# Performance work log

Hardware: AMD Instinct MI355X
Metric: run time of the kernel (lower is better)

Reference implementation:

```python
import jax, jax.numpy as jnp
import numpy as np

K = 5          # k = min(5, min(S, T)) with S = T = 4096
SIGMA = 1.0
EPS_VAR = 1e-08
EPS_LOG = 1e-08


def _entropy(p):
    # sum(-p * log2(clamp(p, 1e-8)), axis=1).mean()
    return jnp.sum(-p * jnp.log2(jnp.clip(p, EPS_LOG, None)), axis=1).mean()


def _pairwise_dist(x):
    # Euclidean cdist via GEMM (matches torch's use_mm_for_euclid path)
    sq = jnp.sum(x * x, axis=1)                       # [N]
    d2 = sq[:, None] + sq[None, :] - 2.0 * (x @ x.T)  # [N, N]
    d2 = jnp.maximum(d2, 0.0)
    # safe sqrt (zero diagonal) — value identical, grad-safe
    return jnp.where(d2 > 0, jnp.sqrt(jnp.where(d2 > 0, d2, 1.0)), 0.0)


def _row_var(block):
    # sqrt(k-th smallest distance per row + eps): max of k smallest
    kth = -jax.lax.top_k(-block, K)[0][:, -1]
    return jnp.sqrt(kth + EPS_VAR)                    # [rows]


def _sim(block, var_row, zero_diag):
    s = jnp.exp(-block / (2.0 * (var_row[:, None] * SIGMA) ** 2))
    if zero_diag:
        n = block.shape[0]
        s = s * (1.0 - jnp.eye(n, dtype=s.dtype))
    return s


def _forward(Feature_all, logit_all, y_source):
    S = y_source.shape[0]
    logit_source = logit_all[:S]
    logit_target = logit_all[S:]

    # cross-entropy on source
    logp = jax.nn.log_softmax(logit_source, axis=1)
    loss_cl = -jnp.take_along_axis(logp, y_source[:, None], axis=1).mean()

    # entropy of target softmax
    loss_ce = _entropy(jax.nn.softmax(logit_target, axis=1))

    # reg_loss_dist
    dist = _pairwise_dist(Feature_all)                # [N, N]
    d_ss = dist[:S, :S]
    d_st = dist[:S, S:]
    d_tt = dist[S:, S:]
    d_ts = dist[S:, :S]

    sim_ss = _sim(d_ss, _row_var(d_ss), True)
    sim_st = _sim(d_st, _row_var(d_st), False)
    sim_tt = _sim(d_tt, _row_var(d_tt), True)
    sim_ts = _sim(d_ts, _row_var(d_ts), False)

    src_intra = jnp.max(sim_ss, axis=1)
    src_inter = jnp.max(sim_st, axis=1)
    tgt_intra = jnp.max(sim_tt, axis=1)
    tgt_inter = jnp.max(sim_ts, axis=1)

    loss_reg = (jnp.abs(src_intra - src_inter).mean()
                + jnp.abs(tgt_intra - tgt_inter).mean())
    return loss_cl, loss_ce, loss_reg


def setup_inputs() -> dict:
    key = jax.random.key(0)
    k1, k2, k3 = jax.random.split(key, 3)
    N, D, C, S = 8192, 256, 65, 4096
    return {
        "Feature_all": jax.random.normal(k1, (N, D), dtype=jnp.float32),
        "logit_all": jax.random.normal(k2, (N, C), dtype=jnp.float32),
        "y_source": jax.random.randint(k3, (S,), 0, C, dtype=jnp.int64
                                       if jax.config.jax_enable_x64 else jnp.int32),
        "device": 0,
    }


def reference(Feature_all, logit_all, y_source, device):
    del device  # torch-specific, ignored
    return _forward(Feature_all, logit_all, y_source)
```

## Files before the change

### kernel.cpp

```cpp
#include <hip/hip_runtime.h>
#include <stdint.h>

#define Nn 8192
#define Dd 256
#define Ss 4096
#define Cc 65

#define TI 128
#define TJ 128
#define BK 32
#define CHUNK 1024
#define NCHUNK (Nn / CHUNK)
#define NJT (CHUNK / TJ)
#define KS (Dd / BK)

#define BIGF 3.0e37f

typedef float f4 __attribute__((ext_vector_type(4)));
typedef __bf16 bf8 __attribute__((ext_vector_type(8)));

__device__ __forceinline__ float wredsum(float v) {
#pragma unroll
  for (int o = 32; o; o >>= 1) v += __shfl_xor(v, o, 64);
  return v;
}
__device__ __forceinline__ float wredmax(float v) {
#pragma unroll
  for (int o = 32; o; o >>= 1) v = fmaxf(v, __shfl_xor(v, o, 64));
  return v;
}

__device__ __forceinline__ unsigned short f2bf(float f) {
  unsigned int u = __float_as_uint(f);
  u = (u + 0x7fffu + ((u >> 16) & 1u)) >> 16;
  return (unsigned short)u;
}

__global__ __launch_bounds__(256) void prep_kernel(const float* __restrict__ X,
                                                   unsigned short* __restrict__ xb,
                                                   float* __restrict__ sqn) {
  int row = blockIdx.x * 4 + (threadIdx.x >> 6);
  int lane = threadIdx.x & 63;
  f4 v = ((const f4*)(X + (size_t)row * Dd))[lane];
  float ss = v[0] * v[0] + v[1] * v[1] + v[2] * v[2] + v[3] * v[3];
  ss = wredsum(ss);
  if (lane == 0) sqn[row] = ss;
  ushort4 o;
  o.x = f2bf(v[0]); o.y = f2bf(v[1]); o.z = f2bf(v[2]); o.w = f2bf(v[3]);
  ((ushort4*)(xb + (size_t)row * Dd))[lane] = o;
}

__device__ __forceinline__ void stage16(const void* g, void* l) {
  __builtin_amdgcn_global_load_lds((__attribute__((address_space(1))) void*)g,
                                   (__attribute__((address_space(3))) void*)l, 16, 0, 0);
}

__global__ __launch_bounds__(256) void dist_kernel(const unsigned short* __restrict__ xb,
                                                   const float* __restrict__ sqn,
                                                   float* __restrict__ top5ws) {
  __shared__ unsigned short ldsA[2][TJ * BK];
  __shared__ unsigned short ldsB[2][TI * BK];

  const int tid = threadIdx.x;
  const int lane = tid & 63;
  const int wv = tid >> 6;
  const int q = lane >> 4;
  const int c = lane & 15;
  const int jw = wv & 1;
  const int iw = wv >> 1;

  const int ib = (blockIdx.x / NCHUNK) * TI;
  const int chunk = blockIdx.x % NCHUNK;
  const int jc0 = chunk * CHUNK;

  const int swz = q ^ ((lane >> 1) & 3);
  const int pr = lane >> 2;
  const int qd = (lane & 3) ^ ((lane >> 3) & 3);
  const int u0 = wv * 2, u1 = wv * 2 + 1;
  const int gcol = qd * 8;

  float top[4][5];
#pragma unroll
  for (int a = 0; a < 4; ++a)
#pragma unroll
    for (int b = 0; b < 5; ++b) top[a][b] = BIGF;

  const int iwbase = ib + iw * 64;

  for (int jt = 0; jt < NJT; ++jt) {
    const int jb = jc0 + jt * TJ;

    f4 acc[4][4];
    f4 z = {0.f, 0.f, 0.f, 0.f};
#pragma unroll
    for (int a = 0; a < 4; ++a)
#pragma unroll
      for (int b2 = 0; b2 < 4; ++b2) acc[a][b2] = z;

    stage16(xb + (size_t)(jb + u0 * 16 + pr) * Dd + gcol, &ldsA[0][u0 * 512]);
    stage16(xb + (size_t)(jb + u1 * 16 + pr) * Dd + gcol, &ldsA[0][u1 * 512]);
    stage16(xb + (size_t)(ib + u0 * 16 + pr) * Dd + gcol, &ldsB[0][u0 * 512]);
    stage16(xb + (size_t)(ib + u1 * 16 + pr) * Dd + gcol, &ldsB[0][u1 * 512]);
    __syncthreads();

#pragma unroll
    for (int ks = 0; ks < KS; ++ks) {
      const int b = ks & 1;
      if (ks + 1 < KS) {
        const int k0 = (ks + 1) * BK;
        stage16(xb + (size_t)(jb + u0 * 16 + pr) * Dd + k0 + gcol, &ldsA[b ^ 1][u0 * 512]);
        stage16(xb + (size_t)(jb + u1 * 16 + pr) * Dd + k0 + gcol, &ldsA[b ^ 1][u1 * 512]);
        stage16(xb + (size_t)(ib + u0 * 16 + pr) * Dd + k0 + gcol, &ldsB[b ^ 1][u0 * 512]);
        stage16(xb + (size_t)(ib + u1 * 16 + pr) * Dd + k0 + gcol, &ldsB[b ^ 1][u1 * 512]);
      }
      bf8 aF[4], bF[4];
#pragma unroll
      for (int rt = 0; rt < 4; ++rt)
        aF[rt] = *(const bf8*)&ldsA[b][(jw * 64 + rt * 16 + c) * 32 + swz * 8];
#pragma unroll
      for (int ct = 0; ct < 4; ++ct)
        bF[ct] = *(const bf8*)&ldsB[b][(iw * 64 + ct * 16 + c) * 32 + swz * 8];
#pragma unroll
      for (int rt = 0; rt < 4; ++rt)
#pragma unroll
        for (int ct = 0; ct < 4; ++ct)
          acc[rt][ct] = __builtin_amdgcn_mfma_f32_16x16x32_bf16(aF[rt], bF[ct], acc[rt][ct], 0, 0, 0);
      __syncthreads();
    }

    const int jrow = jb + jw * 64;
    f4 sq4[4];
#pragma unroll
    for (int rt = 0; rt < 4; ++rt) sq4[rt] = *(const f4*)&sqn[jrow + rt * 16 + q * 4];
    const bool mayDiag = (jrow == iwbase);
#pragma unroll
    for (int ct = 0; ct < 4; ++ct) {
      float t[16];
#pragma unroll
      for (int rt = 0; rt < 4; ++rt)
#pragma unroll
        for (int r = 0; r < 4; ++r)
          t[rt * 4 + r] = fmaf(acc[rt][ct][r], -2.0f, sq4[rt][r]);
      if (mayDiag && ((c >> 2) == q)) t[ct * 4 + (c & 3)] = BIGF;
      float tm = fminf(fminf(fminf(fminf(t[0], t[1]), fminf(t[2], t[3])),
                             fminf(fminf(t[4], t[5]), fminf(t[6], t[7]))),
                       fminf(fminf(fminf(t[8], t[9]), fminf(t[10], t[11])),
                             fminf(fminf(t[12], t[13]), fminf(t[14], t[15]))));
      if (tm < top[ct][4]) {
#pragma unroll
        for (int kk = 0; kk < 16; ++kk) {
          float x = t[kk];
          if (x < top[ct][4]) {
#pragma unroll
            for (int s = 0; s < 4; ++s) {
              float lo = fminf(top[ct][s], x);
              x = fmaxf(top[ct][s], x);
              top[ct][s] = lo;
            }
            top[ct][4] = x;
          }
        }
      }
    }
  }

#pragma unroll
  for (int ct = 0; ct < 4; ++ct) {
    float a0 = top[ct][0], a1 = top[ct][1], a2 = top[ct][2], a3 = top[ct][3], a4 = top[ct][4];
#pragma unroll
    for (int off = 16; off <= 32; off <<= 1) {
      float b0 = __shfl_xor(a0, off, 64);
      float b1 = __shfl_xor(a1, off, 64);
      float b2 = __shfl_xor(a2, off, 64);
      float b3 = __shfl_xor(a3, off, 64);
      float b4 = __shfl_xor(a4, off, 64);
      float c0 = fminf(a0, b0);
      float c1 = fminf(fminf(a1, b1), fmaxf(a0, b0));
      float c2 = fminf(fminf(a2, b2), fminf(fmaxf(a1, b0), fmaxf(a0, b1)));
      float c3 = fminf(fminf(a3, b3), fminf(fmaxf(a2, b0), fminf(fmaxf(a1, b1), fmaxf(a0, b2))));
      float c4 = fminf(fminf(a4, b4),
                       fminf(fmaxf(a3, b0),
                             fminf(fmaxf(a2, b1), fminf(fmaxf(a1, b2), fmaxf(a0, b3)))));
      a0 = c0; a1 = c1; a2 = c2; a3 = c3; a4 = c4;
    }
    if (q == 0) {
      int i = iwbase + ct * 16 + c;
      float* dst = top5ws + ((size_t)i * (NCHUNK * 2) + (chunk * 2 + jw)) * 5;
      dst[0] = a0; dst[1] = a1; dst[2] = a2; dst[3] = a3; dst[4] = a4;
    }
  }
}

__device__ __forceinline__ void merge5(const float* a, const float* b, float* o) {
  o[0] = fminf(a[0], b[0]);
  o[1] = fminf(fminf(a[1], b[1]), fmaxf(a[0], b[0]));
  o[2] = fminf(fminf(a[2], b[2]), fminf(fmaxf(a[1], b[0]), fmaxf(a[0], b[1])));
  o[3] = fminf(fminf(a[3], b[3]), fminf(fmaxf(a[2], b[0]), fminf(fmaxf(a[1], b[1]), fmaxf(a[0], b[2]))));
  o[4] = fminf(fminf(a[4], b[4]),
               fminf(fmaxf(a[3], b[0]),
                     fminf(fmaxf(a[2], b[1]), fminf(fmaxf(a[1], b[2]), fmaxf(a[0], b[3])))));
}

__device__ __forceinline__ void merge8lists(const float* L, float* o) {
  float m01[5], m23[5], m45[5], m67[5], mA[5], mB[5];
  merge5(L + 0, L + 5, m01);
  merge5(L + 10, L + 15, m23);
  merge5(L + 20, L + 25, m45);
  merge5(L + 30, L + 35, m67);
  merge5(m01, m23, mA);
  merge5(m45, m67, mB);
  merge5(mA, mB, o);
}

__global__ __launch_bounds__(256) void reg_kernel(const float* __restrict__ top5ws,
                                                  const float* __restrict__ sqn,
                                                  float* __restrict__ part_reg) {
  int i = blockIdx.x * 256 + threadIdx.x;
  float buf[80];
  const float* L = top5ws + (size_t)i * 80;
#pragma unroll
  for (int k = 0; k < 80; ++k) buf[k] = L[k];
  float mlo[5], mhi[5];
  merge8lists(buf, mlo);
  merge8lists(buf + 40, mhi);
  bool srcRow = (i < Ss);
  float A0 = srcRow ? mlo[0] : mhi[0];
  float A3 = srcRow ? mlo[3] : mhi[3];
  float B0 = srcRow ? mhi[0] : mlo[0];
  float B4 = srcRow ? mhi[4] : mlo[4];
  float sq = sqn[i];
  float dmin_a = sqrtf(fmaxf(A0 + sq, 0.f));
  float kth_a = sqrtf(fmaxf(A3 + sq, 0.f));
  float dmin_b = sqrtf(fmaxf(B0 + sq, 0.f));
  float kth_b = sqrtf(fmaxf(B4 + sq, 0.f));
  float sa = expf(-dmin_a / (2.f * (kth_a + 1e-8f)));
  float sb = expf(-dmin_b / (2.f * (kth_b + 1e-8f)));
  float v = fabsf(sa - sb);
  __shared__ float red[256];
  red[threadIdx.x] = v;
  __syncthreads();
#pragma unroll
  for (int s = 128; s; s >>= 1) {
    if (threadIdx.x < s) red[threadIdx.x] += red[threadIdx.x + s];
    __syncthreads();
  }
  if (threadIdx.x == 0) part_reg[blockIdx.x] = red[0];
}

__global__ __launch_bounds__(256) void loss_kernel(const float* __restrict__ logit,
                                                   const int* __restrict__ y,
                                                   float* __restrict__ part_cl,
                                                   float* __restrict__ part_ce) {
  int row = blockIdx.x * 4 + (threadIdx.x >> 6);
  int lane = threadIdx.x & 63;
  const float* xr = logit + (size_t)row * Cc;
  float x1 = xr[lane];
  float x2 = (lane == 0) ? xr[64] : -BIGF;
  float mx = wredmax(fmaxf(x1, x2));
  float e1 = expf(x1 - mx);
  float e2 = (lane == 0) ? expf(x2 - mx) : 0.f;
  float Z = wredsum(e1 + e2);
  float res;
  if (row < Ss) {
    int yy = y[row];
    float pick = (lane == yy ? x1 : 0.f) + ((lane == 0 && yy == 64) ? x2 : 0.f);
    float xy = wredsum(pick);
    res = -(xy - mx - logf(Z));
  } else {
    float p1 = e1 / Z;
    float t1 = -p1 * log2f(fmaxf(p1, 1e-8f));
    if (lane == 0) {
      float p2 = e2 / Z;
      t1 += -p2 * log2f(fmaxf(p2, 1e-8f));
    }
    res = wredsum(t1);
  }
  __shared__ float a4[4];
  if (lane == 0) a4[threadIdx.x >> 6] = res;
  __syncthreads();
  if (threadIdx.x == 0) {
    float s = a4[0] + a4[1] + a4[2] + a4[3];
    if (blockIdx.x < 1024) part_cl[blockIdx.x] = s;
    else part_ce[blockIdx.x - 1024] = s;
  }
}

__global__ __launch_bounds__(256) void final_kernel(const float* __restrict__ part_cl,
                                                    const float* __restrict__ part_ce,
                                                    const float* __restrict__ part_reg,
                                                    float* __restrict__ out) {
  __shared__ double red[256];
  int tid = threadIdx.x;
  double a = 0.0;
  for (int k = tid; k < 1024; k += 256) a += (double)part_cl[k];
  red[tid] = a; __syncthreads();
  for (int s = 128; s; s >>= 1) { if (tid < s) red[tid] += red[tid + s]; __syncthreads(); }
  double cl = red[0]; __syncthreads();
  a = 0.0;
  for (int k = tid; k < 1024; k += 256) a += (double)part_ce[k];
  red[tid] = a; __syncthreads();
  for (int s = 128; s; s >>= 1) { if (tid < s) red[tid] += red[tid + s]; __syncthreads(); }
  double ce = red[0]; __syncthreads();
  a = (tid < 16) ? (double)part_reg[tid] : 0.0;
  red[tid] = a; __syncthreads();
  for (int s = 128; s; s >>= 1) { if (tid < s) red[tid] += red[tid + s]; __syncthreads(); }
  double rs = red[0]; __syncthreads();
  a = (tid >= 16 && tid < 32) ? (double)part_reg[tid] : 0.0;
  red[tid] = a; __syncthreads();
  for (int s = 128; s; s >>= 1) { if (tid < s) red[tid] += red[tid + s]; __syncthreads(); }
  if (tid == 0) {
    out[0] = (float)(cl / 4096.0);
    out[1] = (float)(ce / 4096.0);
    out[2] = (float)(rs / 4096.0 + red[0] / 4096.0);
  }
}

extern "C" void kernel_launch(void* const* d_in, const int* in_sizes, int n_in,
                              void* d_out, int out_size, void* d_ws, size_t ws_size,
                              hipStream_t stream) {
  (void)in_sizes; (void)n_in; (void)out_size; (void)ws_size;
  const float* X = (const float*)d_in[0];
  const float* logit = (const float*)d_in[1];
  const int* y = (const int*)d_in[2];
  float* out = (float*)d_out;
  char* ws = (char*)d_ws;

  unsigned short* xb = (unsigned short*)ws;
  float* sqn = (float*)(ws + (4u << 20));
  float* top5 = (float*)(ws + (4u << 20) + (64u << 10));
  float* part_cl = (float*)(ws + (7u << 20));
  float* part_ce = part_cl + 1024;
  float* part_reg = part_ce + 1024;

  hipLaunchKernelGGL(prep_kernel, dim3(2048), dim3(256), 0, stream, X, xb, sqn);
  hipLaunchKernelGGL(dist_kernel, dim3((Nn / TI) * NCHUNK), dim3(256), 0, stream, xb, sqn, top5);
  hipLaunchKernelGGL(reg_kernel, dim3(32), dim3(256), 0, stream, top5, sqn, part_reg);
  hipLaunchKernelGGL(loss_kernel, dim3(2048), dim3(256), 0, stream, logit, y, part_cl, part_ce);
  hipLaunchKernelGGL(final_kernel, dim3(1), dim3(256), 0, stream, part_cl, part_ce, part_reg, out);
}
```

Before: 152.8 us.

## Shrink distance chunks, transpose top-5 workspace, fuse reg and loss kernels

Cuts the column chunk of the distance kernel from 1024 to 256, which launches four times as many blocks (2048 instead of 512) to fill the GPU better. The partial top-5 lists are now stored in a list-major layout so per-row merges read coalesced memory, and the merge loops over 32 lists per half instead of 8. The reg and loss kernels are fused into one launch to save a kernel boundary. In exchange, more partial lists are written and merged, and the workspace offsets move to fit the larger buffer.

```diff
diff --git a/kernel.cpp b/kernel.cpp
--- a/kernel.cpp
+++ b/kernel.cpp
@@ -9,10 +9,11 @@
 #define TI 128
 #define TJ 128
 #define BK 32
-#define CHUNK 1024
+#define CHUNK 256
 #define NCHUNK (Nn / CHUNK)
 #define NJT (CHUNK / TJ)
 #define KS (Dd / BK)
+#define NL (NCHUNK * 2)
 
 #define BIGF 3.0e37f
 
@@ -164,6 +165,7 @@
     }
   }
 
+  const int list = chunk * 2 + jw;
 #pragma unroll
   for (int ct = 0; ct < 4; ++ct) {
     float a0 = top[ct][0], a1 = top[ct][1], a2 = top[ct][2], a3 = top[ct][3], a4 = top[ct][4];
@@ -185,103 +187,112 @@
     }
     if (q == 0) {
       int i = iwbase + ct * 16 + c;
-      float* dst = top5ws + ((size_t)i * (NCHUNK * 2) + (chunk * 2 + jw)) * 5;
-      dst[0] = a0; dst[1] = a1; dst[2] = a2; dst[3] = a3; dst[4] = a4;
+      top5ws[(size_t)(list * 5 + 0) * Nn + i] = a0;
+      top5ws[(size_t)(list * 5 + 1) * Nn + i] = a1;
+      top5ws[(size_t)(list * 5 + 2) * Nn + i] = a2;
+      top5ws[(size_t)(list * 5 + 3) * Nn + i] = a3;
+      top5ws[(size_t)(list * 5 + 4) * Nn + i] = a4;
     }
   }
 }
 
 __device__ __forceinline__ void merge5(const float* a, const float* b, float* o) {
-  o[0] = fminf(a[0], b[0]);
-  o[1] = fminf(fminf(a[1], b[1]), fmaxf(a[0], b[0]));
-  o[2] = fminf(fminf(a[2], b[2]), fminf(fmaxf(a[1], b[0]), fmaxf(a[0], b[1])));
-  o[3] = fminf(fminf(a[3], b[3]), fminf(fmaxf(a[2], b[0]), fminf(fmaxf(a[1], b[1]), fmaxf(a[0], b[2]))));
-  o[4] = fminf(fminf(a[4], b[4]),
-               fminf(fmaxf(a[3], b[0]),
-                     fminf(fmaxf(a[2], b[1]), fminf(fmaxf(a[1], b[2]), fmaxf(a[0], b[3])))));
-}
-
-__device__ __forceinline__ void merge8lists(const float* L, float* o) {
-  float m01[5], m23[5], m45[5], m67[5], mA[5], mB[5];
-  merge5(L + 0, L + 5, m01);
-  merge5(L + 10, L + 15, m23);
-  merge5(L + 20, L + 25, m45);
-  merge5(L + 30, L + 35, m67);
-  merge5(m01, m23, mA);
-  merge5(m45, m67, mB);
-  merge5(mA, mB, o);
-}
-
-__global__ __launch_bounds__(256) void reg_kernel(const float* __restrict__ top5ws,
-                                                  const float* __restrict__ sqn,
-                                                  float* __restrict__ part_reg) {
-  int i = blockIdx.x * 256 + threadIdx.x;
-  float buf[80];
-  const float* L = top5ws + (size_t)i * 80;
-#pragma unroll
-  for (int k = 0; k < 80; ++k) buf[k] = L[k];
-  float mlo[5], mhi[5];
-  merge8lists(buf, mlo);
-  merge8lists(buf + 40, mhi);
-  bool srcRow = (i < Ss);
-  float A0 = srcRow ? mlo[0] : mhi[0];
-  float A3 = srcRow ? mlo[3] : mhi[3];
-  float B0 = srcRow ? mhi[0] : mlo[0];
-  float B4 = srcRow ? mhi[4] : mlo[4];
-  float sq = sqn[i];
-  float dmin_a = sqrtf(fmaxf(A0 + sq, 0.f));
-  float kth_a = sqrtf(fmaxf(A3 + sq, 0.f));
-  float dmin_b = sqrtf(fmaxf(B0 + sq, 0.f));
-  float kth_b = sqrtf(fmaxf(B4 + sq, 0.f));
-  float sa = expf(-dmin_a / (2.f * (kth_a + 1e-8f)));
-  float sb = expf(-dmin_b / (2.f * (kth_b + 1e-8f)));
-  float v = fabsf(sa - sb);
+  float t0 = fminf(a[0], b[0]);
+  float t1 = fminf(fminf(a[1], b[1]), fmaxf(a[0], b[0]));
+  float t2 = fminf(fminf(a[2], b[2]), fminf(fmaxf(a[1], b[0]), fmaxf(a[0], b[1])));
+  float t3 = fminf(fminf(a[3], b[3]), fminf(fmaxf(a[2], b[0]), fminf(fmaxf(a[1], b[1]), fmaxf(a[0], b[2]))));
+  float t4 = fminf(fminf(a[4], b[4]),
+                   fminf(fmaxf(a[3], b[0]),
+                         fminf(fmaxf(a[2], b[1]), fminf(fmaxf(a[1], b[2]), fmaxf(a[0], b[3])))));
+  o[0] = t0; o[1] = t1; o[2] = t2; o[3] = t3; o[4] = t4;
+}
+
+__global__ __launch_bounds__(256) void tail_kernel(const float* __restrict__ logit,
+                                                   const int* __restrict__ y,
+                                                   const float* __restrict__ top5ws,
+                                                   const float* __restrict__ sqn,
+                                                   float* __restrict__ part_cl,
+                                                   float* __restrict__ part_ce,
+                                                   float* __restrict__ part_reg) {
   __shared__ float red[256];
-  red[threadIdx.x] = v;
-  __syncthreads();
-#pragma unroll
-  for (int s = 128; s; s >>= 1) {
-    if (threadIdx.x < s) red[threadIdx.x] += red[threadIdx.x + s];
+  const int bx = blockIdx.x;
+  if (bx < 2048) {
+    int row = bx * 4 + (threadIdx.x >> 6);
+    int lane = threadIdx.x & 63;
+    const float* xr = logit + (size_t)row * Cc;
+    float x1 = xr[lane];
+    float x2 = (lane == 0) ? xr[64] : -BIGF;
+    float mx = wredmax(fmaxf(x1, x2));
+    float e1 = expf(x1 - mx);
+    float e2 = (lane == 0) ? expf(x2 - mx) : 0.f;
+    float Z = wredsum(e1 + e2);
+    float res;
+    if (row < Ss) {
+      int yy = y[row];
+      float pick = (lane == yy ? x1 : 0.f) + ((lane == 0 && yy == 64) ? x2 : 0.f);
+      float xy = wredsum(pick);
+      res = -(xy - mx - logf(Z));
+    } else {
+      float p1 = e1 / Z;
+      float t1 = -p1 * log2f(fmaxf(p1, 1e-8f));
+      if (lane == 0) {
+        float p2 = e2 / Z;
+        t1 += -p2 * log2f(fmaxf(p2, 1e-8f));
+      }
+      res = wredsum(t1);
+    }
+    __shared__ float a4[4];
+    if (lane == 0) a4[threadIdx.x >> 6] = res;
     __syncthreads();
-  }
-  if (threadIdx.x == 0) part_reg[blockIdx.x] = red[0];
-}
-
-__global__ __launch_bounds__(256) void loss_kernel(const float* __restrict__ logit,
-                                                   const int* __restrict__ y,
-                                                   float* __restrict__ part_cl,
-                                                   float* __restrict__ part_ce) {
-  int row = blockIdx.x * 4 + (threadIdx.x >> 6);
-  int lane = threadIdx.x & 63;
-  const float* xr = logit + (size_t)row * Cc;
-  float x1 = xr[lane];
-  float x2 = (lane == 0) ? xr[64] : -BIGF;
-  float mx = wredmax(fmaxf(x1, x2));
-  float e1 = expf(x1 - mx);
-  float e2 = (lane == 0) ? expf(x2 - mx) : 0.f;
-  float Z = wredsum(e1 + e2);
-  float res;
-  if (row < Ss) {
-    int yy = y[row];
-    float pick = (lane == yy ? x1 : 0.f) + ((lane == 0 && yy == 64) ? x2 : 0.f);
-    float xy = wredsum(pick);
-    res = -(xy - mx - logf(Z));
+    if (threadIdx.x == 0) {
+      float s = a4[0] + a4[1] + a4[2] + a4[3];
+      if (bx < 1024) part_cl[bx] = s;
+      else part_ce[bx - 1024] = s;
+    }
   } else {
-    float p1 = e1 / Z;
-    float t1 = -p1 * log2f(fmaxf(p1, 1e-8f));
-    if (lane == 0) {
-      float p2 = e2 / Z;
-      t1 += -p2 * log2f(fmaxf(p2, 1e-8f));
-    }
-    res = wredsum(t1);
-  }
-  __shared__ float a4[4];
-  if (lane == 0) a4[threadIdx.x >> 6] = res;
-  __syncthreads();
-  if (threadIdx.x == 0) {
-    float s = a4[0] + a4[1] + a4[2] + a4[3];
-    if (blockIdx.x < 1024) part_cl[blockIdx.x] = s;
-    else part_ce[blockIdx.x - 1024] = s;
+    int i = (bx - 2048) * 256 + threadIdx.x;
+    float mm[2][5];
+#pragma unroll
+    for (int h = 0; h < 2; ++h) {
+      float run[5];
+      int L0 = h * 32;
+#pragma unroll 4
+      for (int k = 0; k < 32; ++k) {
+        float lv[5];
+#pragma unroll
+        for (int s = 0; s < 5; ++s) lv[s] = top5ws[(size_t)((L0 + k) * 5 + s) * Nn + i];
+        if (k == 0) {
+#pragma unroll
+          for (int s = 0; s < 5; ++s) run[s] = lv[s];
+        } else {
+          merge5(run, lv, run);
+        }
+      }
+#pragma unroll
+      for (int s = 0; s < 5; ++s) mm[h][s] = run[s];
+    }
+    bool srcRow = (i < Ss);
+    int hin = srcRow ? 0 : 1, hout = srcRow ? 1 : 0;
+    float A0 = mm[hin][0];
+    float A3 = mm[hin][3];
+    float B0 = mm[hout][0];
+    float B4 = mm[hout][4];
+    float sq = sqn[i];
+    float dmin_a = sqrtf(fmaxf(A0 + sq, 0.f));
+    float kth_a = sqrtf(fmaxf(A3 + sq, 0.f));
+    float dmin_b = sqrtf(fmaxf(B0 + sq, 0.f));
+    float kth_b = sqrtf(fmaxf(B4 + sq, 0.f));
+    float sa = expf(-dmin_a / (2.f * (kth_a + 1e-8f)));
+    float sb = expf(-dmin_b / (2.f * (kth_b + 1e-8f)));
+    float v = fabsf(sa - sb);
+    red[threadIdx.x] = v;
+    __syncthreads();
+#pragma unroll
+    for (int s = 128; s; s >>= 1) {
+      if (threadIdx.x < s) red[threadIdx.x] += red[threadIdx.x + s];
+      __syncthreads();
+    }
+    if (threadIdx.x == 0) part_reg[bx - 2048] = red[0];
   }
 }
 
@@ -301,17 +312,13 @@
   red[tid] = a; __syncthreads();
   for (int s = 128; s; s >>= 1) { if (tid < s) red[tid] += red[tid + s]; __syncthreads(); }
   double ce = red[0]; __syncthreads();
-  a = (tid < 16) ? (double)part_reg[tid] : 0.0;
-  red[tid] = a; __syncthreads();
-  for (int s = 128; s; s >>= 1) { if (tid < s) red[tid] += red[tid + s]; __syncthreads(); }
-  double rs = red[0]; __syncthreads();
-  a = (tid >= 16 && tid < 32) ? (double)part_reg[tid] : 0.0;
+  a = (tid < 32) ? (double)part_reg[tid] : 0.0;
   red[tid] = a; __syncthreads();
   for (int s = 128; s; s >>= 1) { if (tid < s) red[tid] += red[tid + s]; __syncthreads(); }
   if (tid == 0) {
     out[0] = (float)(cl / 4096.0);
     out[1] = (float)(ce / 4096.0);
-    out[2] = (float)(rs / 4096.0 + red[0] / 4096.0);
+    out[2] = (float)(red[0] / 4096.0);
   }
 }
 
@@ -328,13 +335,13 @@
   unsigned short* xb = (unsigned short*)ws;
   float* sqn = (float*)(ws + (4u << 20));
   float* top5 = (float*)(ws + (4u << 20) + (64u << 10));
-  float* part_cl = (float*)(ws + (7u << 20));
+  float* part_cl = (float*)(ws + (16u << 20));
   float* part_ce = part_cl + 1024;
   float* part_reg = part_ce + 1024;
 
   hipLaunchKernelGGL(prep_kernel, dim3(2048), dim3(256), 0, stream, X, xb, sqn);
   hipLaunchKernelGGL(dist_kernel, dim3((Nn / TI) * NCHUNK), dim3(256), 0, stream, xb, sqn, top5);
-  hipLaunchKernelGGL(reg_kernel, dim3(32), dim3(256), 0, stream, top5, sqn, part_reg);
-  hipLaunchKernelGGL(loss_kernel, dim3(2048), dim3(256), 0, stream, logit, y, part_cl, part_ce);
+  hipLaunchKernelGGL(tail_kernel, dim3(2048 + 32), dim3(256), 0, stream,
+                     logit, y, top5, sqn, part_cl, part_ce, part_reg);
   hipLaunchKernelGGL(final_kernel, dim3(1), dim3(256), 0, stream, part_cl, part_ce, part_reg, out);
 }
```

Result: slower. 169.0 us (+10.6%).
